# Performance work log

Hardware: AMD Instinct MI355X
Metric: run time of the kernel (lower is better)

Reference implementation:

```python
import jax, jax.numpy as jnp
import numpy as np

N = 50000
NFEAT = 512
HID = 128
E = 1_600_000


def spmm(row, col, val, dense):
    # sparse [N,N] (COO) @ dense [N,D] -> [N,D]
    gathered = val[:, None] * dense[col]           # [E, D]
    return jax.ops.segment_sum(gathered, row, num_segments=N)


def setup_inputs() -> dict:
    key = jax.random.key(0)
    ks = jax.random.split(key, 12)
    x = jax.random.normal(ks[0], (N, NFEAT), dtype=jnp.float32)
    adj_row = jax.random.randint(ks[1], (E,), 0, N, dtype=jnp.int32)
    adj_col = jax.random.randint(ks[2], (E,), 0, N, dtype=jnp.int32)
    adj_val = jax.random.uniform(ks[3], (E,), dtype=jnp.float32)
    adj_inv_row = jax.random.randint(ks[4], (E,), 0, N, dtype=jnp.int32)
    adj_inv_col = jax.random.randint(ks[5], (E,), 0, N, dtype=jnp.int32)
    adj_inv_val = jax.random.uniform(ks[6], (E,), dtype=jnp.float32)
    # Glorot-ish init for GCN weights
    W1 = jax.random.normal(ks[7], (NFEAT, HID), dtype=jnp.float32) * (1.0 / np.sqrt(NFEAT))
    b1 = jnp.zeros((HID,), dtype=jnp.float32)
    W2 = jax.random.normal(ks[8], (HID, NFEAT), dtype=jnp.float32) * (1.0 / np.sqrt(HID))
    b2 = jnp.zeros((NFEAT,), dtype=jnp.float32)
    return dict(x=x, adj_row=adj_row, adj_col=adj_col, adj_val=adj_val,
                adj_inv_row=adj_inv_row, adj_inv_col=adj_inv_col, adj_inv_val=adj_inv_val,
                W1=W1, b1=b1, W2=W2, b2=b2)


def reference(x, adj_row, adj_col, adj_val, adj_inv_row, adj_inv_col, adj_inv_val,
              W1, b1, W2, b2):
    # Encoder GCN layer: relu( adj @ (x @ W1) + b1 )
    h = jax.nn.relu(spmm(adj_row, adj_col, adj_val, x @ W1) + b1)   # [N, 128]
    embedding = h
    # Decoder GCN layer: relu( adj_inv @ (h @ W2) + b2 )
    out = jax.nn.relu(spmm(adj_inv_row, adj_inv_col, adj_inv_val, h @ W2) + b2)  # [N, nfeat]
    return (out, embedding)
```

## Files before the change

kernel.cpp:

```cpp
#include <hip/hip_runtime.h>

#define NN     50000
#define NFEAT  512
#define HIDD   128
#define NE     1600000
#define NB     ((NN + 255) / 256)
#define NSUB   8

typedef __attribute__((ext_vector_type(8))) short    bf16x8;
typedef __attribute__((ext_vector_type(4))) float    f32x4;
typedef __attribute__((ext_vector_type(4))) unsigned short us4;

__device__ inline unsigned short f2bf(float f) {
  unsigned int u = __float_as_uint(f);
  u += 0x7FFFu + ((u >> 16) & 1u);
  return (unsigned short)(u >> 16);
}

__device__ inline float bf2f(unsigned short h) {
  return __uint_as_float((unsigned int)h << 16);
}

__device__ inline void fma4(float4& a, float v, const float4& d) {
  a.x = fmaf(v, d.x, a.x);
  a.y = fmaf(v, d.y, a.y);
  a.z = fmaf(v, d.z, a.z);
  a.w = fmaf(v, d.w, a.w);
}

__device__ inline void fma4b(float4& a, float v, us4 d) {
  a.x = fmaf(v, bf2f(d[0]), a.x);
  a.y = fmaf(v, bf2f(d[1]), a.y);
  a.z = fmaf(v, bf2f(d[2]), a.z);
  a.w = fmaf(v, bf2f(d[3]), a.w);
}

__global__ __launch_bounds__(256) void hist_rank_kernel(
    const int* __restrict__ rowA, const int* __restrict__ rowB,
    int* __restrict__ cnt8A, int* __restrict__ cnt8B,
    int* __restrict__ rnkA, int* __restrict__ rnkB, int e) {
  const int* row  = blockIdx.y ? rowB : rowA;
  int*       cnt8 = blockIdx.y ? cnt8B : cnt8A;
  int*       rnk  = blockIdx.y ? rnkB : rnkA;
  int i = blockIdx.x * 256 + threadIdx.x;
  if (i < e) {
    int sub = i & (NSUB - 1);
    rnk[i] = atomicAdd(&cnt8[sub * NN + row[i]], 1);
  }
}

__global__ __launch_bounds__(256) void block_sum_kernel(
    const int* __restrict__ cnt8A, const int* __restrict__ cnt8B,
    int* __restrict__ bsumA, int* __restrict__ bsumB, int n) {
  const int* cnt8 = blockIdx.y ? cnt8B : cnt8A;
  int*       bsum = blockIdx.y ? bsumB : bsumA;
  __shared__ int ws[4];
  int i = blockIdx.x * 256 + threadIdx.x;
  int lane = threadIdx.x & 63, wid = threadIdx.x >> 6;
  int v = 0;
  if (i < n) {
#pragma unroll
    for (int s = 0; s < NSUB; ++s) v += cnt8[s * NN + i];
  }
#pragma unroll
  for (int off = 32; off > 0; off >>= 1) v += __shfl_down(v, off, 64);
  if (lane == 0) ws[wid] = v;
  __syncthreads();
  if (threadIdx.x == 0) bsum[blockIdx.x] = ws[0] + ws[1] + ws[2] + ws[3];
}

__global__ __launch_bounds__(256) void scan_partials_kernel(
    int* __restrict__ bsumA, int* __restrict__ bsumB,
    int* __restrict__ rpA, int* __restrict__ rpB, int nb, int nfull) {
  int* bsum   = blockIdx.x ? bsumB : bsumA;
  int* rowptr = blockIdx.x ? rpB : rpA;
  __shared__ int ws[4];
  int t = threadIdx.x;
  int lane = t & 63, wid = t >> 6;
  int v = (t < nb) ? bsum[t] : 0;
  int incl = v;
#pragma unroll
  for (int off = 1; off < 64; off <<= 1) {
    int u = __shfl_up(incl, off, 64);
    if (lane >= off) incl += u;
  }
  if (lane == 63) ws[wid] = incl;
  __syncthreads();
  int wprefix = 0;
  for (int w = 0; w < wid; ++w) wprefix += ws[w];
  incl += wprefix;
  if (t < nb) bsum[t] = incl - v;
  if (t == nb - 1) rowptr[nfull] = incl;
}

__global__ __launch_bounds__(256) void scan_apply_kernel(
    const int* __restrict__ cnt8A, const int* __restrict__ cnt8B,
    const int* __restrict__ bsumA, const int* __restrict__ bsumB,
    int* __restrict__ rpA, int* __restrict__ rpB,
    int* __restrict__ sb8A, int* __restrict__ sb8B, int n) {
  const int* cnt8 = blockIdx.y ? cnt8B : cnt8A;
  const int* bsum = blockIdx.y ? bsumB : bsumA;
  int*       rowptr = blockIdx.y ? rpB : rpA;
  int*       sb8  = blockIdx.y ? sb8B : sb8A;
  __shared__ int ws[4];
  int i = blockIdx.x * 256 + threadIdx.x;
  int lane = threadIdx.x & 63, wid = threadIdx.x >> 6;
  int sc[NSUB];
  int v = 0;
  if (i < n) {
#pragma unroll
    for (int s = 0; s < NSUB; ++s) { sc[s] = cnt8[s * NN + i]; v += sc[s]; }
  }
  int incl = v;
#pragma unroll
  for (int off = 1; off < 64; off <<= 1) {
    int u = __shfl_up(incl, off, 64);
    if (lane >= off) incl += u;
  }
  if (lane == 63) ws[wid] = incl;
  __syncthreads();
  int wprefix = 0;
  for (int w = 0; w < wid; ++w) wprefix += ws[w];
  if (i < n) {
    int base = bsum[blockIdx.x] + wprefix + (incl - v);
    rowptr[i] = base;
#pragma unroll
    for (int s = 0; s < NSUB; ++s) { sb8[s * NN + i] = base; base += sc[s]; }
  }
}

__global__ __launch_bounds__(256) void scatter_rank_kernel(
    const int* __restrict__ rowA, const int* __restrict__ colA,
    const float* __restrict__ valA, const int* __restrict__ rnkA,
    const int* __restrict__ sb8A, int2* __restrict__ pairsA,
    const int* __restrict__ rowB, const int* __restrict__ colB,
    const float* __restrict__ valB, const int* __restrict__ rnkB,
    const int* __restrict__ sb8B, int2* __restrict__ pairsB, int e) {
  const int*   row   = blockIdx.y ? rowB : rowA;
  const int*   col   = blockIdx.y ? colB : colA;
  const float* val   = blockIdx.y ? valB : valA;
  const int*   rnk   = blockIdx.y ? rnkB : rnkA;
  const int*   sb8   = blockIdx.y ? sb8B : sb8A;
  int2*        pairs = blockIdx.y ? pairsB : pairsA;
  int i = blockIdx.x * 256 + threadIdx.x;
  if (i < e) {
    int sub = i & (NSUB - 1);
    int p = sb8[sub * NN + row[i]] + rnk[i];
    pairs[p] = make_int2(col[i], __float_as_int(val[i]));
  }
}

template <bool DB16, bool EPI, bool WF32, bool WB16>
__global__ __launch_bounds__(256) void spmm_kernel(
    const int* __restrict__ rowptr, const int2* __restrict__ pairs,
    const void* __restrict__ dense, const float* __restrict__ bias,
    float* __restrict__ outf, unsigned short* __restrict__ outb, int n) {
  int r = blockIdx.x * 8 + (threadIdx.x >> 5);
  if (r >= n) return;
  int c4 = (threadIdx.x & 31);
  int s = rowptr[r], e = rowptr[r + 1];
  float4 a0 = make_float4(0.f, 0.f, 0.f, 0.f);
  float4 a1 = a0, a2 = a0, a3 = a0;
  int j = s;
  if constexpr (DB16) {
    const unsigned short* d16 = (const unsigned short*)dense;
    for (; j + 8 <= e; j += 8) {
      int2 p0 = pairs[j + 0], p1 = pairs[j + 1], p2 = pairs[j + 2], p3 = pairs[j + 3];
      int2 p4 = pairs[j + 4], p5 = pairs[j + 5], p6 = pairs[j + 6], p7 = pairs[j + 7];
      us4 d0 = *(const us4*)(d16 + (size_t)p0.x * 128 + c4 * 4);
      us4 d1 = *(const us4*)(d16 + (size_t)p1.x * 128 + c4 * 4);
      us4 d2 = *(const us4*)(d16 + (size_t)p2.x * 128 + c4 * 4);
      us4 d3 = *(const us4*)(d16 + (size_t)p3.x * 128 + c4 * 4);
      us4 d4 = *(const us4*)(d16 + (size_t)p4.x * 128 + c4 * 4);
      us4 d5 = *(const us4*)(d16 + (size_t)p5.x * 128 + c4 * 4);
      us4 d6 = *(const us4*)(d16 + (size_t)p6.x * 128 + c4 * 4);
      us4 d7 = *(const us4*)(d16 + (size_t)p7.x * 128 + c4 * 4);
      fma4b(a0, __int_as_float(p0.y), d0);
      fma4b(a1, __int_as_float(p1.y), d1);
      fma4b(a2, __int_as_float(p2.y), d2);
      fma4b(a3, __int_as_float(p3.y), d3);
      fma4b(a0, __int_as_float(p4.y), d4);
      fma4b(a1, __int_as_float(p5.y), d5);
      fma4b(a2, __int_as_float(p6.y), d6);
      fma4b(a3, __int_as_float(p7.y), d7);
    }
    for (; j < e; ++j) {
      int2 ev = pairs[j];
      us4 d = *(const us4*)(d16 + (size_t)ev.x * 128 + c4 * 4);
      fma4b(a0, __int_as_float(ev.y), d);
    }
  } else {
    const float4* dense4 = (const float4*)dense;
    for (; j + 8 <= e; j += 8) {
      int2 p0 = pairs[j + 0], p1 = pairs[j + 1], p2 = pairs[j + 2], p3 = pairs[j + 3];
      int2 p4 = pairs[j + 4], p5 = pairs[j + 5], p6 = pairs[j + 6], p7 = pairs[j + 7];
      float4 d0 = dense4[(size_t)p0.x * 32 + c4];
      float4 d1 = dense4[(size_t)p1.x * 32 + c4];
      float4 d2 = dense4[(size_t)p2.x * 32 + c4];
      float4 d3 = dense4[(size_t)p3.x * 32 + c4];
      float4 d4 = dense4[(size_t)p4.x * 32 + c4];
      float4 d5 = dense4[(size_t)p5.x * 32 + c4];
      float4 d6 = dense4[(size_t)p6.x * 32 + c4];
      float4 d7 = dense4[(size_t)p7.x * 32 + c4];
      fma4(a0, __int_as_float(p0.y), d0);
      fma4(a1, __int_as_float(p1.y), d1);
      fma4(a2, __int_as_float(p2.y), d2);
      fma4(a3, __int_as_float(p3.y), d3);
      fma4(a0, __int_as_float(p4.y), d4);
      fma4(a1, __int_as_float(p5.y), d5);
      fma4(a2, __int_as_float(p6.y), d6);
      fma4(a3, __int_as_float(p7.y), d7);
    }
    for (; j < e; ++j) {
      int2 ev = pairs[j];
      float4 d = dense4[(size_t)ev.x * 32 + c4];
      fma4(a0, __int_as_float(ev.y), d);
    }
  }
  float4 acc;
  acc.x = (a0.x + a1.x) + (a2.x + a3.x);
  acc.y = (a0.y + a1.y) + (a2.y + a3.y);
  acc.z = (a0.z + a1.z) + (a2.z + a3.z);
  acc.w = (a0.w + a1.w) + (a2.w + a3.w);
  if (EPI) {
    float4 b = ((const float4*)bias)[c4];
    acc.x = fmaxf(acc.x + b.x, 0.f);
    acc.y = fmaxf(acc.y + b.y, 0.f);
    acc.z = fmaxf(acc.z + b.z, 0.f);
    acc.w = fmaxf(acc.w + b.w, 0.f);
  }
  if (WF32)
    *(float4*)(outf + (size_t)r * 128 + c4 * 4) = acc;
  if (WB16) {
    us4 h = {f2bf(acc.x), f2bf(acc.y), f2bf(acc.z), f2bf(acc.w)};
    *(us4*)(outb + (size_t)r * 128 + c4 * 4) = h;
  }
}

template <int K, int N, bool EPI, bool ABF16, bool OUTB>
__global__ __launch_bounds__(256) void gemm_mfma_kernel(
    const void* __restrict__ Av, const float* __restrict__ B,
    const float* __restrict__ bias, void* __restrict__ Cv, int M) {
  __shared__ __align__(16) unsigned short Alds[4096];
  __shared__ __align__(16) unsigned short Blds[4096];
  int tid = threadIdx.x;
  int lane = tid & 63, wid = tid >> 6;
  int wm = wid >> 1, wn = wid & 1;
  int rowBase = blockIdx.x * 128;
  int colBase = blockIdx.y * 128;
  int kg = tid & 7, mrow = tid >> 3;
  int aquad = kg >> 1, aj0 = (kg & 1) * 4;
  int bn = tid & 127, kh = tid >> 7;
  int NTb = bn >> 4, nloc = bn & 15;

  f32x4 acc[4][4];
#pragma unroll
  for (int mt = 0; mt < 4; ++mt)
#pragma unroll
    for (int nt = 0; nt < 4; ++nt)
      acc[mt][nt] = (f32x4){0.f, 0.f, 0.f, 0.f};

  for (int kb = 0; kb < K; kb += 32) {
    float4 av[4];
    us4 av16[4];
    if constexpr (ABF16) {
      const unsigned short* A = (const unsigned short*)Av;
#pragma unroll
      for (int p = 0; p < 4; ++p) {
        int r = rowBase + p * 32 + mrow;
        av16[p] = (r < M) ? *(const us4*)(A + (size_t)r * K + kb + kg * 4)
                          : (us4){0, 0, 0, 0};
      }
    } else {
      const float* A = (const float*)Av;
#pragma unroll
      for (int p = 0; p < 4; ++p) {
        int r = rowBase + p * 32 + mrow;
        av[p] = (r < M) ? *(const float4*)(A + (size_t)r * K + kb + kg * 4)
                        : make_float4(0.f, 0.f, 0.f, 0.f);
      }
    }
    float bv[4][4];
#pragma unroll
    for (int p = 0; p < 4; ++p) {
      int k = p * 8 + kh * 4;
#pragma unroll
      for (int i = 0; i < 4; ++i)
        bv[p][i] = B[(size_t)(kb + k + i) * N + colBase + bn];
    }
    __syncthreads();
#pragma unroll
    for (int p = 0; p < 4; ++p) {
      int m = p * 32 + mrow;
      int MT = m >> 4, mloc = m & 15;
      us4 h;
      if constexpr (ABF16) h = av16[p];
      else h = (us4){f2bf(av[p].x), f2bf(av[p].y), f2bf(av[p].z), f2bf(av[p].w)};
      *(us4*)&Alds[(((MT * 4 + aquad) * 16 + mloc) << 3) + aj0] = h;
    }
#pragma unroll
    for (int p = 0; p < 4; ++p) {
      us4 h = {f2bf(bv[p][0]), f2bf(bv[p][1]), f2bf(bv[p][2]), f2bf(bv[p][3])};
      *(us4*)&Blds[(((NTb * 4 + p) * 16 + nloc) << 3) + kh * 4] = h;
    }
    __syncthreads();
    bf16x8 af[4], bf[4];
#pragma unroll
    for (int mt = 0; mt < 4; ++mt)
      af[mt] = *(bf16x8*)&Alds[(((wm * 4 + mt) * 64 + lane)) << 3];
#pragma unroll
    for (int nt = 0; nt < 4; ++nt)
      bf[nt] = *(bf16x8*)&Blds[(((wn * 4 + nt) * 64 + lane)) << 3];
#pragma unroll
    for (int mt = 0; mt < 4; ++mt)
#pragma unroll
      for (int nt = 0; nt < 4; ++nt)
        acc[mt][nt] = __builtin_amdgcn_mfma_f32_16x16x32_bf16(
            af[mt], bf[nt], acc[mt][nt], 0, 0, 0);
  }
  int cquad = lane >> 4, cn = lane & 15;
#pragma unroll
  for (int nt = 0; nt < 4; ++nt) {
    int col = colBase + wn * 64 + nt * 16 + cn;
    float bb = EPI ? bias[col] : 0.f;
#pragma unroll
    for (int mt = 0; mt < 4; ++mt) {
      int r0 = rowBase + wm * 64 + mt * 16 + cquad * 4;
#pragma unroll
      for (int i = 0; i < 4; ++i) {
        int r = r0 + i;
        if (r < M) {
          float o = acc[mt][nt][i];
          if (EPI) o = fmaxf(o + bb, 0.f);
          if constexpr (OUTB)
            ((unsigned short*)Cv)[(size_t)r * N + col] = f2bf(o);
          else
            ((float*)Cv)[(size_t)r * N + col] = o;
        }
      }
    }
  }
}

extern "C" void kernel_launch(void* const* d_in, const int* in_sizes, int n_in,
                              void* d_out, int out_size, void* d_ws, size_t ws_size,
                              hipStream_t stream) {
  const float* x        = (const float*)d_in[0];
  const int*   adj_row  = (const int*)d_in[1];
  const int*   adj_col  = (const int*)d_in[2];
  const float* adj_val  = (const float*)d_in[3];
  const int*   ainv_row = (const int*)d_in[4];
  const int*   ainv_col = (const int*)d_in[5];
  const float* ainv_val = (const float*)d_in[6];
  const float* W1       = (const float*)d_in[7];
  const float* b1       = (const float*)d_in[8];
  const float* W2       = (const float*)d_in[9];
  const float* b2       = (const float*)d_in[10];

  float* out = (float*)d_out;
  float* emb = out + (size_t)NN * NFEAT;

  size_t off = 0;
  auto carve = [&](size_t bytes) {
    void* p = (char*)d_ws + off;
    off += (bytes + 255) & ~(size_t)255;
    return p;
  };
  unsigned short* Tb   = (unsigned short*)carve((size_t)NN * HIDD * 2);
  unsigned short* H0b  = (unsigned short*)carve((size_t)NN * HIDD * 2);
  int*  rowptr_a = (int*)carve(50004 * 4);
  int*  rowptr_b = (int*)carve(50004 * 4);
  int*  cnt8_a   = (int*)carve((size_t)NSUB * NN * 4);
  int*  cnt8_b   = (int*)carve((size_t)NSUB * NN * 4);
  int*  sb8_a    = (int*)carve((size_t)NSUB * NN * 4);
  int*  sb8_b    = (int*)carve((size_t)NSUB * NN * 4);
  int*  bsum_a   = (int*)carve(256 * 4);
  int*  bsum_b   = (int*)carve(256 * 4);
  int*  rank_a   = (int*)carve((size_t)NE * 4);
  int*  rank_b   = (int*)carve((size_t)NE * 4);
  int2* pairs_a  = (int2*)carve((size_t)NE * 8);
  int2* pairs_b  = (int2*)carve((size_t)NE * 8);
  unsigned short* embb = (unsigned short*)((char*)d_ws + off);
  bool full = ws_size >= off + (size_t)NN * HIDD * 2;

  hipMemsetAsync(cnt8_a, 0, (size_t)NSUB * NN * sizeof(int), stream);
  hipMemsetAsync(cnt8_b, 0, (size_t)NSUB * NN * sizeof(int), stream);
  hist_rank_kernel<<<dim3(NE / 256, 2), 256, 0, stream>>>(
      adj_row, ainv_row, cnt8_a, cnt8_b, rank_a, rank_b, NE);
  block_sum_kernel<<<dim3(NB, 2), 256, 0, stream>>>(cnt8_a, cnt8_b, bsum_a, bsum_b, NN);
  scan_partials_kernel<<<2, 256, 0, stream>>>(bsum_a, bsum_b, rowptr_a, rowptr_b,
                                              NB, NN);
  scan_apply_kernel<<<dim3(NB, 2), 256, 0, stream>>>(
      cnt8_a, cnt8_b, bsum_a, bsum_b, rowptr_a, rowptr_b, sb8_a, sb8_b, NN);
  scatter_rank_kernel<<<dim3(NE / 256, 2), 256, 0, stream>>>(
      adj_row, adj_col, adj_val, rank_a, sb8_a, pairs_a,
      ainv_row, ainv_col, ainv_val, rank_b, sb8_b, pairs_b, NE);

  gemm_mfma_kernel<NFEAT, HIDD, false, false, true>
      <<<dim3((NN + 127) / 128, 1), 256, 0, stream>>>(x, W1, nullptr, H0b, NN);

  if (full)
    spmm_kernel<true, true, true, true><<<(NN + 7) / 8, 256, 0, stream>>>(
        rowptr_a, pairs_a, H0b, b1, emb, embb, NN);
  else
    spmm_kernel<true, true, true, false><<<(NN + 7) / 8, 256, 0, stream>>>(
        rowptr_a, pairs_a, H0b, b1, emb, nullptr, NN);

  if (full)
    spmm_kernel<true, false, false, true><<<(NN + 7) / 8, 256, 0, stream>>>(
        rowptr_b, pairs_b, embb, nullptr, nullptr, Tb, NN);
  else
    spmm_kernel<false, false, false, true><<<(NN + 7) / 8, 256, 0, stream>>>(
        rowptr_b, pairs_b, emb, nullptr, nullptr, Tb, NN);

  gemm_mfma_kernel<HIDD, NFEAT, true, true, false>
      <<<dim3((NN + 127) / 128, 4), 256, 0, stream>>>(Tb, W2, b2, out, NN);
}
```

Before: 634.6 us.

## Replace global-atomic COO-to-CSR build with per-chunk LDS histograms

The CSR build now splits the edges into 64 chunks. Each chunk counts its rows in a shared-memory histogram of packed 16-bit counters and writes that histogram out. Per-chunk, per-row base offsets come from a scan, and a second pass recomputes local ranks with LDS atomics to scatter the pairs. This drops the global atomics, the rank array and the memsets. The cost is that only 128 blocks run (low occupancy with 100KB of LDS each), each per-row scan reads 64 counts, and a 12.8MB base array must be written and read back.

```diff
diff --git a/kernel.cpp b/kernel.cpp
--- a/kernel.cpp
+++ b/kernel.cpp
@@ -5,7 +5,9 @@
 #define HIDD   128
 #define NE     1600000
 #define NB     ((NN + 255) / 256)
-#define NSUB   8
+#define NCH    64
+#define CHSZ   (NE / NCH)
+#define NWRD   (NN / 2)
 
 typedef __attribute__((ext_vector_type(8))) short    bf16x8;
 typedef __attribute__((ext_vector_type(4))) float    f32x4;
@@ -35,32 +37,39 @@
   a.w = fmaf(v, bf2f(d[3]), a.w);
 }
 
-__global__ __launch_bounds__(256) void hist_rank_kernel(
+__global__ __launch_bounds__(256) void chunk_hist_kernel(
     const int* __restrict__ rowA, const int* __restrict__ rowB,
-    int* __restrict__ cnt8A, int* __restrict__ cnt8B,
-    int* __restrict__ rnkA, int* __restrict__ rnkB, int e) {
-  const int* row  = blockIdx.y ? rowB : rowA;
-  int*       cnt8 = blockIdx.y ? cnt8B : cnt8A;
-  int*       rnk  = blockIdx.y ? rnkB : rnkA;
-  int i = blockIdx.x * 256 + threadIdx.x;
-  if (i < e) {
-    int sub = i & (NSUB - 1);
-    rnk[i] = atomicAdd(&cnt8[sub * NN + row[i]], 1);
-  }
+    unsigned int* __restrict__ cntA, unsigned int* __restrict__ cntB) {
+  __shared__ unsigned int lcnt[NWRD];
+  const int*    row = blockIdx.y ? rowB : rowA;
+  unsigned int* cnt = blockIdx.y ? cntB : cntA;
+  int b = blockIdx.x;
+  for (int w = threadIdx.x; w < NWRD; w += 256) lcnt[w] = 0;
+  __syncthreads();
+  int base = b * CHSZ;
+  for (int j = threadIdx.x; j < CHSZ; j += 256) {
+    int r = row[base + j];
+    atomicAdd(&lcnt[r >> 1], 1u << ((r & 1) * 16));
+  }
+  __syncthreads();
+  unsigned int* dst = cnt + (size_t)b * NWRD;
+  for (int w = threadIdx.x; w < NWRD; w += 256) dst[w] = lcnt[w];
 }
 
 __global__ __launch_bounds__(256) void block_sum_kernel(
-    const int* __restrict__ cnt8A, const int* __restrict__ cnt8B,
+    const unsigned int* __restrict__ cntA, const unsigned int* __restrict__ cntB,
     int* __restrict__ bsumA, int* __restrict__ bsumB, int n) {
-  const int* cnt8 = blockIdx.y ? cnt8B : cnt8A;
-  int*       bsum = blockIdx.y ? bsumB : bsumA;
+  const unsigned int* cnt = blockIdx.y ? cntB : cntA;
+  int*                bsum = blockIdx.y ? bsumB : bsumA;
   __shared__ int ws[4];
   int i = blockIdx.x * 256 + threadIdx.x;
   int lane = threadIdx.x & 63, wid = threadIdx.x >> 6;
   int v = 0;
   if (i < n) {
-#pragma unroll
-    for (int s = 0; s < NSUB; ++s) v += cnt8[s * NN + i];
+    const unsigned int* cw = cnt + (i >> 1);
+    int sh = (i & 1) * 16;
+    for (int b = 0; b < NCH; ++b)
+      v += (int)((cw[(size_t)b * NWRD] >> sh) & 0xFFFFu);
   }
 #pragma unroll
   for (int off = 32; off > 0; off >>= 1) v += __shfl_down(v, off, 64);
@@ -94,22 +103,24 @@
 }
 
 __global__ __launch_bounds__(256) void scan_apply_kernel(
-    const int* __restrict__ cnt8A, const int* __restrict__ cnt8B,
+    const unsigned int* __restrict__ cntA, const unsigned int* __restrict__ cntB,
     const int* __restrict__ bsumA, const int* __restrict__ bsumB,
     int* __restrict__ rpA, int* __restrict__ rpB,
-    int* __restrict__ sb8A, int* __restrict__ sb8B, int n) {
-  const int* cnt8 = blockIdx.y ? cnt8B : cnt8A;
+    int* __restrict__ baseA, int* __restrict__ baseB, int n) {
+  const unsigned int* cnt = blockIdx.y ? cntB : cntA;
   const int* bsum = blockIdx.y ? bsumB : bsumA;
   int*       rowptr = blockIdx.y ? rpB : rpA;
-  int*       sb8  = blockIdx.y ? sb8B : sb8A;
+  int*       base32 = blockIdx.y ? baseB : baseA;
   __shared__ int ws[4];
   int i = blockIdx.x * 256 + threadIdx.x;
   int lane = threadIdx.x & 63, wid = threadIdx.x >> 6;
-  int sc[NSUB];
-  int v = 0;
+  int v = 0, sh = 0;
+  const unsigned int* cw = nullptr;
   if (i < n) {
-#pragma unroll
-    for (int s = 0; s < NSUB; ++s) { sc[s] = cnt8[s * NN + i]; v += sc[s]; }
+    cw = cnt + (i >> 1);
+    sh = (i & 1) * 16;
+    for (int b = 0; b < NCH; ++b)
+      v += (int)((cw[(size_t)b * NWRD] >> sh) & 0xFFFFu);
   }
   int incl = v;
 #pragma unroll
@@ -122,30 +133,39 @@
   int wprefix = 0;
   for (int w = 0; w < wid; ++w) wprefix += ws[w];
   if (i < n) {
-    int base = bsum[blockIdx.x] + wprefix + (incl - v);
-    rowptr[i] = base;
-#pragma unroll
-    for (int s = 0; s < NSUB; ++s) { sb8[s * NN + i] = base; base += sc[s]; }
-  }
-}
-
-__global__ __launch_bounds__(256) void scatter_rank_kernel(
+    int run = bsum[blockIdx.x] + wprefix + (incl - v);
+    rowptr[i] = run;
+    for (int b = 0; b < NCH; ++b) {
+      base32[(size_t)b * NN + i] = run;
+      run += (int)((cw[(size_t)b * NWRD] >> sh) & 0xFFFFu);
+    }
+  }
+}
+
+__global__ __launch_bounds__(256) void scatter_chunk_kernel(
     const int* __restrict__ rowA, const int* __restrict__ colA,
-    const float* __restrict__ valA, const int* __restrict__ rnkA,
-    const int* __restrict__ sb8A, int2* __restrict__ pairsA,
+    const float* __restrict__ valA, const int* __restrict__ baseA,
+    int2* __restrict__ pairsA,
     const int* __restrict__ rowB, const int* __restrict__ colB,
-    const float* __restrict__ valB, const int* __restrict__ rnkB,
-    const int* __restrict__ sb8B, int2* __restrict__ pairsB, int e) {
-  const int*   row   = blockIdx.y ? rowB : rowA;
-  const int*   col   = blockIdx.y ? colB : colA;
-  const float* val   = blockIdx.y ? valB : valA;
-  const int*   rnk   = blockIdx.y ? rnkB : rnkA;
-  const int*   sb8   = blockIdx.y ? sb8B : sb8A;
-  int2*        pairs = blockIdx.y ? pairsB : pairsA;
-  int i = blockIdx.x * 256 + threadIdx.x;
-  if (i < e) {
-    int sub = i & (NSUB - 1);
-    int p = sb8[sub * NN + row[i]] + rnk[i];
+    const float* __restrict__ valB, const int* __restrict__ baseB,
+    int2* __restrict__ pairsB) {
+  __shared__ unsigned int lcnt[NWRD];
+  const int*   row    = blockIdx.y ? rowB : rowA;
+  const int*   col    = blockIdx.y ? colB : colA;
+  const float* val    = blockIdx.y ? valB : valA;
+  const int*   base32 = blockIdx.y ? baseB : baseA;
+  int2*        pairs  = blockIdx.y ? pairsB : pairsA;
+  int b = blockIdx.x;
+  for (int w = threadIdx.x; w < NWRD; w += 256) lcnt[w] = 0;
+  __syncthreads();
+  int base = b * CHSZ;
+  const int* bslice = base32 + (size_t)b * NN;
+  for (int j = threadIdx.x; j < CHSZ; j += 256) {
+    int i = base + j;
+    int r = row[i];
+    int sh = (r & 1) * 16;
+    int lr = (int)((atomicAdd(&lcnt[r >> 1], 1u << sh) >> sh) & 0xFFFFu);
+    int p = bslice[r] + lr;
     pairs[p] = make_int2(col[i], __float_as_int(val[i]));
   }
 }
@@ -370,31 +390,27 @@
   unsigned short* H0b  = (unsigned short*)carve((size_t)NN * HIDD * 2);
   int*  rowptr_a = (int*)carve(50004 * 4);
   int*  rowptr_b = (int*)carve(50004 * 4);
-  int*  cnt8_a   = (int*)carve((size_t)NSUB * NN * 4);
-  int*  cnt8_b   = (int*)carve((size_t)NSUB * NN * 4);
-  int*  sb8_a    = (int*)carve((size_t)NSUB * NN * 4);
-  int*  sb8_b    = (int*)carve((size_t)NSUB * NN * 4);
+  unsigned int* cnt_a = (unsigned int*)carve((size_t)NCH * NWRD * 4);
+  unsigned int* cnt_b = (unsigned int*)carve((size_t)NCH * NWRD * 4);
+  int*  base_a   = (int*)carve((size_t)NCH * NN * 4);
+  int*  base_b   = (int*)carve((size_t)NCH * NN * 4);
   int*  bsum_a   = (int*)carve(256 * 4);
   int*  bsum_b   = (int*)carve(256 * 4);
-  int*  rank_a   = (int*)carve((size_t)NE * 4);
-  int*  rank_b   = (int*)carve((size_t)NE * 4);
   int2* pairs_a  = (int2*)carve((size_t)NE * 8);
   int2* pairs_b  = (int2*)carve((size_t)NE * 8);
   unsigned short* embb = (unsigned short*)((char*)d_ws + off);
   bool full = ws_size >= off + (size_t)NN * HIDD * 2;
 
-  hipMemsetAsync(cnt8_a, 0, (size_t)NSUB * NN * sizeof(int), stream);
-  hipMemsetAsync(cnt8_b, 0, (size_t)NSUB * NN * sizeof(int), stream);
-  hist_rank_kernel<<<dim3(NE / 256, 2), 256, 0, stream>>>(
-      adj_row, ainv_row, cnt8_a, cnt8_b, rank_a, rank_b, NE);
-  block_sum_kernel<<<dim3(NB, 2), 256, 0, stream>>>(cnt8_a, cnt8_b, bsum_a, bsum_b, NN);
+  chunk_hist_kernel<<<dim3(NCH, 2), 256, 0, stream>>>(
+      adj_row, ainv_row, cnt_a, cnt_b);
+  block_sum_kernel<<<dim3(NB, 2), 256, 0, stream>>>(cnt_a, cnt_b, bsum_a, bsum_b, NN);
   scan_partials_kernel<<<2, 256, 0, stream>>>(bsum_a, bsum_b, rowptr_a, rowptr_b,
                                               NB, NN);
   scan_apply_kernel<<<dim3(NB, 2), 256, 0, stream>>>(
-      cnt8_a, cnt8_b, bsum_a, bsum_b, rowptr_a, rowptr_b, sb8_a, sb8_b, NN);
-  scatter_rank_kernel<<<dim3(NE / 256, 2), 256, 0, stream>>>(
-      adj_row, adj_col, adj_val, rank_a, sb8_a, pairs_a,
-      ainv_row, ainv_col, ainv_val, rank_b, sb8_b, pairs_b, NE);
+      cnt_a, cnt_b, bsum_a, bsum_b, rowptr_a, rowptr_b, base_a, base_b, NN);
+  scatter_chunk_kernel<<<dim3(NCH, 2), 256, 0, stream>>>(
+      adj_row, adj_col, adj_val, base_a, pairs_a,
+      ainv_row, ainv_col, ainv_val, base_b, pairs_b);
 
   gemm_mfma_kernel<NFEAT, HIDD, false, false, true>
       <<<dim3((NN + 127) / 128, 1), 256, 0, stream>>>(x, W1, nullptr, H0b, NN);
```

After: 628.0 us. No clear change (-1.0%).
